# Optimization experiments

Hardware: AMD Instinct MI355X
Metric: run time of the kernel (lower is better)

Reference implementation:

```python
import jax, jax.numpy as jnp
import numpy as np

TAU = 0.07
K = 50
EPS = 1e-8


def _flat_norm(x):
    # [B, C, H, W] -> [B*H*W, C], L2-normalized along C
    B, C = x.shape[0], x.shape[1]
    x = jnp.moveaxis(x, 1, -1).reshape(-1, C)
    n = jnp.linalg.norm(x, axis=-1, keepdims=True)
    return x / jnp.maximum(n, 1e-12)


def setup_inputs() -> dict:
    key = jax.random.key(0)
    ks = jax.random.split(key, 5)
    shp = (2, 128, 64, 64)
    lshp = (2, 4, 64, 64)
    return {
        "input": jax.random.normal(ks[0], shp, dtype=jnp.float32),
        "positive": jax.random.normal(ks[1], shp, dtype=jnp.float32),
        "negative": jax.random.normal(ks[2], shp, dtype=jnp.float32),
        "input_logits": jax.random.normal(ks[3], lshp, dtype=jnp.float32),
        "negative_logits": jax.random.normal(ks[4], lshp, dtype=jnp.float32),
    }


def reference(input, positive, negative, input_logits, negative_logits):
    norm_input = _flat_norm(input)        # [N, C]
    norm_positive = _flat_norm(positive)  # [N, C]
    norm_negative = _flat_norm(negative)  # [N, C]

    # check_input: multi-class logits branch (softmax over class dim, then max)
    in_probs = jax.nn.softmax(input_logits, axis=1)
    neg_probs = jax.nn.softmax(negative_logits, axis=1)
    seg_input = jnp.argmax(in_probs, axis=1).reshape(-1)       # [N] int
    seg_negative = jnp.argmax(neg_probs, axis=1).reshape(-1)   # [N] int
    negative_prob = jnp.max(neg_probs, axis=1).reshape(-1)     # [N] float

    # positive cosine similarity (unit vectors -> dot product)
    pos_sim = jnp.sum(norm_input * norm_positive, axis=-1)     # [N]

    # mask[i, j] = (seg_input[j] != seg_negative[i]) * negative_prob[i]
    diff = (seg_input[None, :] != seg_negative[:, None]).astype(jnp.float16)
    masked = diff.astype(jnp.float32) * negative_prob[:, None]  # [N, N]

    # top-k over dim=0 (negatives) for each input column j -> indices [N, K]
    _, idx = jax.lax.top_k(masked.T, K)                         # [N, K]
    sampled = norm_negative[idx]                                # [N, K, C]

    neg_sim = jnp.einsum('nkc,nc->nk', sampled, norm_input)     # [N, K]
    nominator = jnp.exp(pos_sim / TAU)                          # [N]
    denominator = jnp.sum(jnp.exp(neg_sim / TAU), axis=1) + nominator
    loss = -jnp.mean(jnp.log(nominator / (denominator + EPS)))

    alter_sim = jnp.einsum('nkc,nc->nk', sampled, norm_positive)
    alter_den = jnp.sum(jnp.exp(alter_sim / TAU), axis=1) + nominator
    alter_loss = -jnp.mean(jnp.log(nominator / (alter_den + EPS)))

    return loss + alter_loss
```

## Files before the change

kernel.cpp:

```cpp
#include <hip/hip_runtime.h>
#include <math.h>

#define TAU_INV (1.0f / 0.07f)
#define KSEL 50
#define KPAD 64
#define NPIX 8192
#define CCH 128
#define HWSZ 4096
#define NCLS 4
#define EPSL 1e-8f
#define NBINS 1026
#define PXT 32
#define SROW 132

__global__ void __launch_bounds__(256) prep_kernel(
        const float* __restrict__ input, const float* __restrict__ positive,
        const float* __restrict__ negative,
        const float* __restrict__ ilog, const float* __restrict__ nlog,
        float* __restrict__ ni, float* __restrict__ np_,
        float* __restrict__ nnsel,
        int* __restrict__ perm, int* __restrict__ cnt,
        float* __restrict__ out) {
    __shared__ union {
        struct {
            float tile[CCH][65];
            float partial[4][64];
            float invn[64];
        } a;
        struct {
            unsigned hist[NBINS];
            unsigned coarse[33];
            unsigned long long cand[2048];
            unsigned wsum[4];
            int topk_l[KPAD];
            unsigned above_cnt, cand_cnt;
            int sB, sc0;
        } b;
    } sm;

    int t = threadIdx.x;
    int bid = blockIdx.x;

    if (bid == 0 && t == 0) out[0] = 0.0f;

    if (bid >= NCLS) {
        int blk = bid - NCLS;
        int tensor = blk >> 7, chunk = blk & 127;
        const float* src = (tensor == 0) ? input : positive;
        float*       dst = (tensor == 0) ? ni    : np_;

        int n0 = chunk * 64;
        int b = n0 >> 12, hw0 = n0 & (HWSZ - 1);
        const float* base = src + (size_t)b * CCH * HWSZ + hw0;

        #pragma unroll
        for (int i = 0; i < 8; ++i) {
            int lin = t + i * 256;
            int cc = lin >> 4, hwq = (lin & 15) * 4;
            float4 v = *(const float4*)&base[(size_t)cc * HWSZ + hwq];
            sm.a.tile[cc][hwq + 0] = v.x; sm.a.tile[cc][hwq + 1] = v.y;
            sm.a.tile[cc][hwq + 2] = v.z; sm.a.tile[cc][hwq + 3] = v.w;
        }
        __syncthreads();

        int nof = t & 63, part = t >> 6;
        float s = 0.f;
        #pragma unroll
        for (int j = 0; j < 32; ++j) {
            float v = sm.a.tile[part * 32 + j][nof];
            s += v * v;
        }
        sm.a.partial[part][nof] = s;
        __syncthreads();
        if (t < 64) {
            float tot = sm.a.partial[0][t] + sm.a.partial[1][t] +
                        sm.a.partial[2][t] + sm.a.partial[3][t];
            sm.a.invn[t] = 1.0f / fmaxf(sqrtf(tot), 1e-12f);
        }
        __syncthreads();

        #pragma unroll
        for (int i = 0; i < 8; ++i) {
            int lin = t + i * 256;
            int nf = lin >> 5, cq = (lin & 31) * 4;
            float inv = sm.a.invn[nf];
            float4 o;
            o.x = sm.a.tile[cq + 0][nf] * inv;
            o.y = sm.a.tile[cq + 1][nf] * inv;
            o.z = sm.a.tile[cq + 2][nf] * inv;
            o.w = sm.a.tile[cq + 3][nf] * inv;
            *(float4*)&dst[(size_t)(n0 + nf) * CCH + cq] = o;
        }
        return;
    }

    int c = bid;

    for (int i = t; i < NBINS; i += 256) sm.b.hist[i] = 0;
    if (t < 33) sm.b.coarse[t] = 0;
    if (t == 0) { sm.b.above_cnt = 0; sm.b.cand_cnt = 0; }
    __syncthreads();

    unsigned keys[32];
    unsigned mask = 0u;
    #pragma unroll
    for (int s = 0; s < 8; ++s) {
        int i4 = (t + s * 256) * 4;
        int b = i4 >> 12, hw = i4 & (HWSZ - 1);

        const float* pi = ilog + (size_t)b * NCLS * HWSZ + hw;
        float4 a0 = *(const float4*)&pi[0];
        float4 a1 = *(const float4*)&pi[HWSZ];
        float4 a2 = *(const float4*)&pi[2 * HWSZ];
        float4 a3 = *(const float4*)&pi[3 * HWSZ];
        const float* pn = nlog + (size_t)b * NCLS * HWSZ + hw;
        float4 b0 = *(const float4*)&pn[0];
        float4 b1 = *(const float4*)&pn[HWSZ];
        float4 b2 = *(const float4*)&pn[2 * HWSZ];
        float4 b3 = *(const float4*)&pn[3 * HWSZ];

        const float* A0 = (const float*)&a0; const float* A1 = (const float*)&a1;
        const float* A2 = (const float*)&a2; const float* A3 = (const float*)&a3;
        const float* B0 = (const float*)&b0; const float* B1 = (const float*)&b1;
        const float* B2 = (const float*)&b2; const float* B3 = (const float*)&b3;
        #pragma unroll
        for (int j = 0; j < 4; ++j) {
            float l0 = A0[j], l1 = A1[j], l2 = A2[j], l3 = A3[j];
            int bi = 0; float bv = l0;
            if (l1 > bv) { bv = l1; bi = 1; }
            if (l2 > bv) { bv = l2; bi = 2; }
            if (l3 > bv) { bv = l3; bi = 3; }
            if (bi == c) mask |= (1u << (s * 4 + j));
            float m0 = B0[j], m1 = B1[j], m2 = B2[j], m3 = B3[j];
            int ci = 0; float cv = m0;
            if (m1 > cv) { cv = m1; ci = 1; }
            if (m2 > cv) { cv = m2; ci = 2; }
            if (m3 > cv) { cv = m3; ci = 3; }
            float ssum = expf(m0 - cv) + expf(m1 - cv) + expf(m2 - cv) + expf(m3 - cv);
            float npv = 1.0f / ssum;

            float v = (ci != c) ? npv : 0.0f;
            unsigned key = __float_as_uint(v);
            keys[s * 4 + j] = key;
            int bin = (key < 0x3E800000u) ? 0 : (int)(1u + ((key - 0x3E800000u) >> 14));
            atomicAdd(&sm.b.hist[bin], 1u);
        }
    }

    {
        int cnt_t = __popc(mask);
        int lane = t & 63, wv = t >> 6;
        int x = cnt_t;
        #pragma unroll
        for (int off = 1; off < 64; off <<= 1) {
            int o = __shfl_up(x, off);
            if (lane >= off) x += o;
        }
        if (lane == 63) sm.b.wsum[wv] = (unsigned)x;
        __syncthreads();
        int base = x - cnt_t;
        for (int ww = 0; ww < wv; ++ww) base += (int)sm.b.wsum[ww];
        unsigned mm = mask; int k = 0;
        while (mm) {
            int bit = __ffs(mm) - 1; mm &= (mm - 1);
            int s2 = bit >> 2, j2 = bit & 3;
            perm[c * NPIX + base + k] = (t + s2 * 256) * 4 + j2;
            ++k;
        }
        if (t == 0) cnt[c] = (int)(sm.b.wsum[0] + sm.b.wsum[1] +
                                   sm.b.wsum[2] + sm.b.wsum[3]);
    }
    __syncthreads();

    for (int i = t; i < NBINS; i += 256) atomicAdd(&sm.b.coarse[i >> 5], sm.b.hist[i]);
    __syncthreads();

    if (t == 0) {
        unsigned cum = 0; int j = 32;
        for (; j > 0; --j) {
            unsigned h = sm.b.coarse[j];
            if (cum + h >= KSEL) break;
            cum += h;
        }
        int hi = j * 32 + 31; if (hi > NBINS - 1) hi = NBINS - 1;
        int B = 0;
        for (int b = hi; b >= j * 32; --b) {
            unsigned h = sm.b.hist[b];
            if (cum + h >= KSEL) { B = b; break; }
            cum += h;
        }
        sm.b.sB = B; sm.b.sc0 = (int)cum;
    }
    __syncthreads();
    int B = sm.b.sB, c0 = sm.b.sc0;

    #pragma unroll
    for (int s = 0; s < 8; ++s) {
        #pragma unroll
        for (int j = 0; j < 4; ++j) {
            unsigned key = keys[s * 4 + j];
            int bin = (key < 0x3E800000u) ? 0 : (int)(1u + ((key - 0x3E800000u) >> 14));
            int i = (t + s * 256) * 4 + j;
            if (bin > B) {
                unsigned pos = atomicAdd(&sm.b.above_cnt, 1u);
                sm.b.topk_l[pos] = i;
            } else if (bin == B) {
                unsigned jj = atomicAdd(&sm.b.cand_cnt, 1u);
                if (jj < 2048)
                    sm.b.cand[jj] = ((unsigned long long)key << 32) |
                                    (unsigned long long)(0xFFFFFFFFu - (unsigned)i);
            }
        }
    }
    __syncthreads();

    int m = KSEL - c0;
    int cb = (int)sm.b.cand_cnt; if (cb > 2048) cb = 2048;
    if (t < 64) {
        for (int r = 0; r < m; ++r) {
            unsigned long long best = 0;
            for (int j = t; j < cb; j += 64) {
                unsigned long long v = sm.b.cand[j];
                if (v > best) best = v;
            }
            #pragma unroll
            for (int off = 32; off; off >>= 1) {
                unsigned long long o = __shfl_xor(best, off);
                if (o > best) best = o;
            }
            if (t == 0) sm.b.topk_l[c0 + r] =
                (int)(0xFFFFFFFFu - (unsigned)(best & 0xFFFFFFFFull));
            for (int j = t; j < cb; j += 64)
                if (sm.b.cand[j] == best) sm.b.cand[j] = 0;
        }
    }
    __syncthreads();

    {
        int row = t >> 2;
        int ch0 = (t & 3) * 32;
        if (row < KSEL) {
            int px = sm.b.topk_l[row];
            int b = px >> 12, hw = px & (HWSZ - 1);
            const float* src = negative + (size_t)b * CCH * HWSZ + hw;
            float vals[32]; float ss = 0.f;
            #pragma unroll
            for (int k2 = 0; k2 < 32; ++k2) {
                float v = src[(size_t)(ch0 + k2) * HWSZ];
                vals[k2] = v; ss += v * v;
            }
            ss += __shfl_xor(ss, 1);
            ss += __shfl_xor(ss, 2);
            float inv = 1.0f / fmaxf(sqrtf(ss), 1e-12f);
            float* dst = nnsel + (size_t)(c * KSEL + row) * CCH + ch0;
            #pragma unroll
            for (int k2 = 0; k2 < 32; ++k2) dst[k2] = vals[k2] * inv;
        }
    }
}

__global__ void __launch_bounds__(256) loss_kernel(
        const float* __restrict__ ni, const float* __restrict__ npos,
        const float* __restrict__ nnsel,
        const int* __restrict__ perm, const int* __restrict__ cnt,
        float* __restrict__ out) {
    __shared__ float Sl[KPAD * SROW];
    __shared__ float Xl[PXT * SROW];
    __shared__ float Pl[PXT * SROW];
    __shared__ float bsum[4];

    int c = blockIdx.y;
    int count = cnt[c];
    int start = blockIdx.x * PXT;
    if (start >= count) return;
    int t = threadIdx.x;

    {
        int row = t >> 2;
        int ch0 = (t & 3) * 32;
        float* dst = &Sl[row * SROW + ch0];
        if (row < KSEL) {
            const float* src = nnsel + (size_t)(c * KSEL + row) * CCH + ch0;
            #pragma unroll
            for (int i = 0; i < 8; ++i)
                ((float4*)dst)[i] = ((const float4*)src)[i];
        } else {
            float4 z = make_float4(0.f, 0.f, 0.f, 0.f);
            #pragma unroll
            for (int i = 0; i < 8; ++i)
                ((float4*)dst)[i] = z;
        }
    }
    {
        int row = t >> 3;
        int slot = start + row;
        int px = perm[c * NPIX + ((slot < count) ? slot : start)];
        int ch0 = (t & 7) * 16;
        const float* sx = ni + (size_t)px * CCH + ch0;
        const float* sp = npos + (size_t)px * CCH + ch0;
        float* dx = &Xl[row * SROW + ch0];
        float* dp = &Pl[row * SROW + ch0];
        #pragma unroll
        for (int i = 0; i < 4; ++i) {
            ((float4*)dx)[i] = ((const float4*)sx)[i];
            ((float4*)dp)[i] = ((const float4*)sp)[i];
        }
    }
    __syncthreads();

    int ktid = t & 7, pxid = t >> 3;
    float acc_i[8] = {0.f, 0.f, 0.f, 0.f, 0.f, 0.f, 0.f, 0.f};
    float acc_p[8] = {0.f, 0.f, 0.f, 0.f, 0.f, 0.f, 0.f, 0.f};
    float ps = 0.f;
    const float* Xr = &Xl[pxid * SROW];
    const float* Pr = &Pl[pxid * SROW];

    #pragma unroll 2
    for (int ch = 0; ch < CCH; ch += 4) {
        float4 xv = *(const float4*)&Xr[ch];
        float4 pv = *(const float4*)&Pr[ch];
        ps += xv.x * pv.x + xv.y * pv.y + xv.z * pv.z + xv.w * pv.w;
        #pragma unroll
        for (int r = 0; r < 8; ++r) {
            float4 sv = *(const float4*)&Sl[(ktid + r * 8) * SROW + ch];
            acc_i[r] += sv.x * xv.x + sv.y * xv.y + sv.z * xv.z + sv.w * xv.w;
            acc_p[r] += sv.x * pv.x + sv.y * pv.y + sv.z * pv.z + sv.w * pv.w;
        }
    }

    float si = 0.f, spp = 0.f;
    #pragma unroll
    for (int r = 0; r < 8; ++r) {
        si  += expf(acc_i[r] * TAU_INV);
        spp += expf(acc_p[r] * TAU_INV);
    }
    #pragma unroll
    for (int off = 1; off < 8; off <<= 1) {
        si  += __shfl_xor(si, off);
        spp += __shfl_xor(spp, off);
    }

    float v = 0.f;
    if (ktid == 0 && (start + pxid) < count) {
        si  -= (float)(KPAD - KSEL);
        spp -= (float)(KPAD - KSEL);
        float nom = expf(ps * TAU_INV);
        float li = -logf(nom / (si + nom + EPSL));
        float lp = -logf(nom / (spp + nom + EPSL));
        v = (li + lp) * (1.0f / (float)NPIX);
    }
    v += __shfl_xor(v, 8);
    v += __shfl_xor(v, 16);
    v += __shfl_xor(v, 32);
    int w = t >> 6;
    if ((t & 63) == 0) bsum[w] = v;
    __syncthreads();
    if (t == 0) atomicAdd(out, bsum[0] + bsum[1] + bsum[2] + bsum[3]);
}

extern "C" void kernel_launch(void* const* d_in, const int* in_sizes, int n_in,
                              void* d_out, int out_size, void* d_ws, size_t ws_size,
                              hipStream_t stream) {
    const float* input      = (const float*)d_in[0];
    const float* positive   = (const float*)d_in[1];
    const float* negative   = (const float*)d_in[2];
    const float* in_logits  = (const float*)d_in[3];
    const float* neg_logits = (const float*)d_in[4];
    float* out = (float*)d_out;

    float* ws    = (float*)d_ws;
    float* ni    = ws;
    float* np_   = ws + 1048576;
    float* nnsel = ws + 2097152;
    int*   cnt   = (int*)(ws + 3145728);
    int*   perm  = cnt + 64;

    prep_kernel<<<256 + NCLS, 256, 0, stream>>>(input, positive, negative,
                                                in_logits, neg_logits,
                                                ni, np_, nnsel, perm, cnt, out);
    dim3 lgrid(NPIX / PXT, NCLS);
    loss_kernel<<<lgrid, 256, 0, stream>>>(ni, np_, nnsel, perm, cnt, out);
}
```

Baseline: 109.6 us.

## Fuse input/positive normalization into loss kernel and widen top-k blocks

Removes the separate normalization pass that wrote L2-normalized copies of input and positive to workspace. The loss kernel now gathers raw NCHW values for its selected pixels and normalizes them in registers with a shuffle reduction. This removes a full intermediate write and re-read. The top-k kernel now runs one 1024-thread block per class, with more threads sharing the histogram, scan and negative gather. The trade-off is strided, less coalesced channel reads from NCHW in the loss kernel.

```diff
diff --git a/kernel.cpp b/kernel.cpp
--- a/kernel.cpp
+++ b/kernel.cpp
@@ -13,99 +13,32 @@
 #define PXT 32
 #define SROW 132
 
-__global__ void __launch_bounds__(256) prep_kernel(
-        const float* __restrict__ input, const float* __restrict__ positive,
+__global__ void __launch_bounds__(1024) topk_kernel(
+        const float* __restrict__ ilog, const float* __restrict__ nlog,
         const float* __restrict__ negative,
-        const float* __restrict__ ilog, const float* __restrict__ nlog,
-        float* __restrict__ ni, float* __restrict__ np_,
-        float* __restrict__ nnsel,
-        int* __restrict__ perm, int* __restrict__ cnt,
+        float* __restrict__ nnsel, int* __restrict__ perm, int* __restrict__ cnt,
         float* __restrict__ out) {
-    __shared__ union {
-        struct {
-            float tile[CCH][65];
-            float partial[4][64];
-            float invn[64];
-        } a;
-        struct {
-            unsigned hist[NBINS];
-            unsigned coarse[33];
-            unsigned long long cand[2048];
-            unsigned wsum[4];
-            int topk_l[KPAD];
-            unsigned above_cnt, cand_cnt;
-            int sB, sc0;
-        } b;
-    } sm;
-
-    int t = threadIdx.x;
-    int bid = blockIdx.x;
-
-    if (bid == 0 && t == 0) out[0] = 0.0f;
-
-    if (bid >= NCLS) {
-        int blk = bid - NCLS;
-        int tensor = blk >> 7, chunk = blk & 127;
-        const float* src = (tensor == 0) ? input : positive;
-        float*       dst = (tensor == 0) ? ni    : np_;
-
-        int n0 = chunk * 64;
-        int b = n0 >> 12, hw0 = n0 & (HWSZ - 1);
-        const float* base = src + (size_t)b * CCH * HWSZ + hw0;
-
-        #pragma unroll
-        for (int i = 0; i < 8; ++i) {
-            int lin = t + i * 256;
-            int cc = lin >> 4, hwq = (lin & 15) * 4;
-            float4 v = *(const float4*)&base[(size_t)cc * HWSZ + hwq];
-            sm.a.tile[cc][hwq + 0] = v.x; sm.a.tile[cc][hwq + 1] = v.y;
-            sm.a.tile[cc][hwq + 2] = v.z; sm.a.tile[cc][hwq + 3] = v.w;
-        }
-        __syncthreads();
-
-        int nof = t & 63, part = t >> 6;
-        float s = 0.f;
-        #pragma unroll
-        for (int j = 0; j < 32; ++j) {
-            float v = sm.a.tile[part * 32 + j][nof];
-            s += v * v;
-        }
-        sm.a.partial[part][nof] = s;
-        __syncthreads();
-        if (t < 64) {
-            float tot = sm.a.partial[0][t] + sm.a.partial[1][t] +
-                        sm.a.partial[2][t] + sm.a.partial[3][t];
-            sm.a.invn[t] = 1.0f / fmaxf(sqrtf(tot), 1e-12f);
-        }
-        __syncthreads();
-
-        #pragma unroll
-        for (int i = 0; i < 8; ++i) {
-            int lin = t + i * 256;
-            int nf = lin >> 5, cq = (lin & 31) * 4;
-            float inv = sm.a.invn[nf];
-            float4 o;
-            o.x = sm.a.tile[cq + 0][nf] * inv;
-            o.y = sm.a.tile[cq + 1][nf] * inv;
-            o.z = sm.a.tile[cq + 2][nf] * inv;
-            o.w = sm.a.tile[cq + 3][nf] * inv;
-            *(float4*)&dst[(size_t)(n0 + nf) * CCH + cq] = o;
-        }
-        return;
-    }
-
-    int c = bid;
-
-    for (int i = t; i < NBINS; i += 256) sm.b.hist[i] = 0;
-    if (t < 33) sm.b.coarse[t] = 0;
-    if (t == 0) { sm.b.above_cnt = 0; sm.b.cand_cnt = 0; }
-    __syncthreads();
-
-    unsigned keys[32];
+    __shared__ unsigned hist[NBINS];
+    __shared__ unsigned coarse[33];
+    __shared__ unsigned long long cand[2048];
+    __shared__ unsigned wsum[16];
+    __shared__ int topk_l[KPAD];
+    __shared__ unsigned above_cnt, cand_cnt;
+    __shared__ int sB, sc0;
+
+    int c = blockIdx.x, t = threadIdx.x;
+    if (c == 0 && t == 0) out[0] = 0.0f;
+
+    for (int i = t; i < NBINS; i += 1024) hist[i] = 0;
+    if (t < 33) coarse[t] = 0;
+    if (t == 0) { above_cnt = 0; cand_cnt = 0; }
+    __syncthreads();
+
+    unsigned keys[8];
     unsigned mask = 0u;
     #pragma unroll
-    for (int s = 0; s < 8; ++s) {
-        int i4 = (t + s * 256) * 4;
+    for (int s = 0; s < 2; ++s) {
+        int i4 = (t * 2 + s) * 4;
         int b = i4 >> 12, hw = i4 & (HWSZ - 1);
 
         const float* pi = ilog + (size_t)b * NCLS * HWSZ + hw;
@@ -131,6 +64,7 @@
             if (l2 > bv) { bv = l2; bi = 2; }
             if (l3 > bv) { bv = l3; bi = 3; }
             if (bi == c) mask |= (1u << (s * 4 + j));
+
             float m0 = B0[j], m1 = B1[j], m2 = B2[j], m3 = B3[j];
             int ci = 0; float cv = m0;
             if (m1 > cv) { cv = m1; ci = 1; }
@@ -143,7 +77,7 @@
             unsigned key = __float_as_uint(v);
             keys[s * 4 + j] = key;
             int bin = (key < 0x3E800000u) ? 0 : (int)(1u + ((key - 0x3E800000u) >> 14));
-            atomicAdd(&sm.b.hist[bin], 1u);
+            atomicAdd(&hist[bin], 1u);
         }
     }
 
@@ -156,71 +90,72 @@
             int o = __shfl_up(x, off);
             if (lane >= off) x += o;
         }
-        if (lane == 63) sm.b.wsum[wv] = (unsigned)x;
+        if (lane == 63) wsum[wv] = (unsigned)x;
         __syncthreads();
         int base = x - cnt_t;
-        for (int ww = 0; ww < wv; ++ww) base += (int)sm.b.wsum[ww];
-        unsigned mm = mask; int k = 0;
+        for (int ww = 0; ww < wv; ++ww) base += (int)wsum[ww];
+        unsigned mm = mask;
         while (mm) {
             int bit = __ffs(mm) - 1; mm &= (mm - 1);
-            int s2 = bit >> 2, j2 = bit & 3;
-            perm[c * NPIX + base + k] = (t + s2 * 256) * 4 + j2;
-            ++k;
-        }
-        if (t == 0) cnt[c] = (int)(sm.b.wsum[0] + sm.b.wsum[1] +
-                                   sm.b.wsum[2] + sm.b.wsum[3]);
-    }
-    __syncthreads();
-
-    for (int i = t; i < NBINS; i += 256) atomicAdd(&sm.b.coarse[i >> 5], sm.b.hist[i]);
+            perm[c * NPIX + base] = t * 8 + bit;
+            ++base;
+        }
+        if (t == 0) {
+            int tot = 0;
+            for (int w2 = 0; w2 < 16; ++w2) tot += (int)wsum[w2];
+            cnt[c] = tot;
+        }
+    }
+
+    for (int i = t; i < NBINS; i += 1024) atomicAdd(&coarse[i >> 5], hist[i]);
     __syncthreads();
 
     if (t == 0) {
         unsigned cum = 0; int j = 32;
         for (; j > 0; --j) {
-            unsigned h = sm.b.coarse[j];
+            unsigned h = coarse[j];
             if (cum + h >= KSEL) break;
             cum += h;
         }
         int hi = j * 32 + 31; if (hi > NBINS - 1) hi = NBINS - 1;
         int B = 0;
         for (int b = hi; b >= j * 32; --b) {
-            unsigned h = sm.b.hist[b];
+            unsigned h = hist[b];
             if (cum + h >= KSEL) { B = b; break; }
             cum += h;
         }
-        sm.b.sB = B; sm.b.sc0 = (int)cum;
-    }
-    __syncthreads();
-    int B = sm.b.sB, c0 = sm.b.sc0;
+        sB = B; sc0 = (int)cum;
+    }
+    __syncthreads();
+    int B = sB, c0 = sc0;
 
     #pragma unroll
-    for (int s = 0; s < 8; ++s) {
+    for (int s = 0; s < 2; ++s) {
         #pragma unroll
         for (int j = 0; j < 4; ++j) {
             unsigned key = keys[s * 4 + j];
             int bin = (key < 0x3E800000u) ? 0 : (int)(1u + ((key - 0x3E800000u) >> 14));
-            int i = (t + s * 256) * 4 + j;
+            int i = t * 8 + s * 4 + j;
             if (bin > B) {
-                unsigned pos = atomicAdd(&sm.b.above_cnt, 1u);
-                sm.b.topk_l[pos] = i;
+                unsigned pos = atomicAdd(&above_cnt, 1u);
+                topk_l[pos] = i;
             } else if (bin == B) {
-                unsigned jj = atomicAdd(&sm.b.cand_cnt, 1u);
+                unsigned jj = atomicAdd(&cand_cnt, 1u);
                 if (jj < 2048)
-                    sm.b.cand[jj] = ((unsigned long long)key << 32) |
-                                    (unsigned long long)(0xFFFFFFFFu - (unsigned)i);
+                    cand[jj] = ((unsigned long long)key << 32) |
+                               (unsigned long long)(0xFFFFFFFFu - (unsigned)i);
             }
         }
     }
     __syncthreads();
 
     int m = KSEL - c0;
-    int cb = (int)sm.b.cand_cnt; if (cb > 2048) cb = 2048;
+    int cb = (int)cand_cnt; if (cb > 2048) cb = 2048;
     if (t < 64) {
         for (int r = 0; r < m; ++r) {
             unsigned long long best = 0;
             for (int j = t; j < cb; j += 64) {
-                unsigned long long v = sm.b.cand[j];
+                unsigned long long v = cand[j];
                 if (v > best) best = v;
             }
             #pragma unroll
@@ -228,39 +163,41 @@
                 unsigned long long o = __shfl_xor(best, off);
                 if (o > best) best = o;
             }
-            if (t == 0) sm.b.topk_l[c0 + r] =
+            if (t == 0) topk_l[c0 + r] =
                 (int)(0xFFFFFFFFu - (unsigned)(best & 0xFFFFFFFFull));
             for (int j = t; j < cb; j += 64)
-                if (sm.b.cand[j] == best) sm.b.cand[j] = 0;
+                if (cand[j] == best) cand[j] = 0;
         }
     }
     __syncthreads();
 
     {
-        int row = t >> 2;
-        int ch0 = (t & 3) * 32;
+        int row = t >> 4;
+        int ch0 = (t & 15) * 8;
         if (row < KSEL) {
-            int px = sm.b.topk_l[row];
+            int px = topk_l[row];
             int b = px >> 12, hw = px & (HWSZ - 1);
             const float* src = negative + (size_t)b * CCH * HWSZ + hw;
-            float vals[32]; float ss = 0.f;
-            #pragma unroll
-            for (int k2 = 0; k2 < 32; ++k2) {
-                float v = src[(size_t)(ch0 + k2) * HWSZ];
-                vals[k2] = v; ss += v * v;
+            float vals[8]; float ss = 0.f;
+            #pragma unroll
+            for (int k = 0; k < 8; ++k) {
+                float v = src[(size_t)(ch0 + k) * HWSZ];
+                vals[k] = v; ss += v * v;
             }
             ss += __shfl_xor(ss, 1);
             ss += __shfl_xor(ss, 2);
+            ss += __shfl_xor(ss, 4);
+            ss += __shfl_xor(ss, 8);
             float inv = 1.0f / fmaxf(sqrtf(ss), 1e-12f);
             float* dst = nnsel + (size_t)(c * KSEL + row) * CCH + ch0;
             #pragma unroll
-            for (int k2 = 0; k2 < 32; ++k2) dst[k2] = vals[k2] * inv;
+            for (int k = 0; k < 8; ++k) dst[k] = vals[k] * inv;
         }
     }
 }
 
 __global__ void __launch_bounds__(256) loss_kernel(
-        const float* __restrict__ ni, const float* __restrict__ npos,
+        const float* __restrict__ input, const float* __restrict__ positive,
         const float* __restrict__ nnsel,
         const int* __restrict__ perm, const int* __restrict__ cnt,
         float* __restrict__ out) {
@@ -295,15 +232,34 @@
         int row = t >> 3;
         int slot = start + row;
         int px = perm[c * NPIX + ((slot < count) ? slot : start)];
+        int b = px >> 12, hw = px & (HWSZ - 1);
         int ch0 = (t & 7) * 16;
-        const float* sx = ni + (size_t)px * CCH + ch0;
-        const float* sp = npos + (size_t)px * CCH + ch0;
+        const float* bx = input    + (size_t)b * CCH * HWSZ + hw;
+        const float* bp = positive + (size_t)b * CCH * HWSZ + hw;
+        float xv[16], pv[16];
+        float ssx = 0.f, ssp = 0.f;
+        #pragma unroll
+        for (int k = 0; k < 16; ++k) {
+            float vx = bx[(size_t)(ch0 + k) * HWSZ];
+            float vp = bp[(size_t)(ch0 + k) * HWSZ];
+            xv[k] = vx; ssx += vx * vx;
+            pv[k] = vp; ssp += vp * vp;
+        }
+        ssx += __shfl_xor(ssx, 1); ssp += __shfl_xor(ssp, 1);
+        ssx += __shfl_xor(ssx, 2); ssp += __shfl_xor(ssp, 2);
+        ssx += __shfl_xor(ssx, 4); ssp += __shfl_xor(ssp, 4);
+        float ix = 1.0f / fmaxf(sqrtf(ssx), 1e-12f);
+        float ip = 1.0f / fmaxf(sqrtf(ssp), 1e-12f);
         float* dx = &Xl[row * SROW + ch0];
         float* dp = &Pl[row * SROW + ch0];
         #pragma unroll
         for (int i = 0; i < 4; ++i) {
-            ((float4*)dx)[i] = ((const float4*)sx)[i];
-            ((float4*)dp)[i] = ((const float4*)sp)[i];
+            float4 ox = make_float4(xv[4*i+0]*ix, xv[4*i+1]*ix,
+                                    xv[4*i+2]*ix, xv[4*i+3]*ix);
+            float4 op = make_float4(pv[4*i+0]*ip, pv[4*i+1]*ip,
+                                    pv[4*i+2]*ip, pv[4*i+3]*ip);
+            ((float4*)dx)[i] = ox;
+            ((float4*)dp)[i] = op;
         }
     }
     __syncthreads();
@@ -369,15 +325,13 @@
     float* out = (float*)d_out;
 
     float* ws    = (float*)d_ws;
-    float* ni    = ws;
-    float* np_   = ws + 1048576;
-    float* nnsel = ws + 2097152;
-    int*   cnt   = (int*)(ws + 3145728);
+    float* nnsel = ws;
+    int*   cnt   = (int*)(ws + 32768);
     int*   perm  = cnt + 64;
 
-    prep_kernel<<<256 + NCLS, 256, 0, stream>>>(input, positive, negative,
-                                                in_logits, neg_logits,
-                                                ni, np_, nnsel, perm, cnt, out);
+    topk_kernel<<<NCLS, 1024, 0, stream>>>(in_logits, neg_logits, negative,
+                                           nnsel, perm, cnt, out);
     dim3 lgrid(NPIX / PXT, NCLS);
-    loss_kernel<<<lgrid, 256, 0, stream>>>(ni, np_, nnsel, perm, cnt, out);
+    loss_kernel<<<lgrid, 256, 0, stream>>>(input, positive, nnsel,
+                                           perm, cnt, out);
 }
```

Measured after the change: 104.2 us. 1.05x faster.

## Widen prep blocks to 1024 threads to shorten per-class top-k critical path

Applied to the files above, without the earlier changes.

Launches prep_kernel with 1024 threads per block. The four per-class selection blocks now handle 8 pixels per thread instead of 32, and the negative gather uses 16 threads per row instead of 4. The normalization blocks simply idle 768 of their threads. The workspace offset for cnt/perm moves closer to nnsel. This targets the serial latency of the few class blocks that dominate prep, at the cost of wasted threads in the 256 normalization blocks and lower occupancy per CU.

```diff
diff --git a/kernel.cpp b/kernel.cpp
--- a/kernel.cpp
+++ b/kernel.cpp
@@ -13,7 +13,7 @@
 #define PXT 32
 #define SROW 132
 
-__global__ void __launch_bounds__(256) prep_kernel(
+__global__ void __launch_bounds__(1024) prep_kernel(
         const float* __restrict__ input, const float* __restrict__ positive,
         const float* __restrict__ negative,
         const float* __restrict__ ilog, const float* __restrict__ nlog,
@@ -31,7 +31,7 @@
             unsigned hist[NBINS];
             unsigned coarse[33];
             unsigned long long cand[2048];
-            unsigned wsum[4];
+            unsigned wsum[16];
             int topk_l[KPAD];
             unsigned above_cnt, cand_cnt;
             int sB, sc0;
@@ -41,8 +41,6 @@
     int t = threadIdx.x;
     int bid = blockIdx.x;
 
-    if (bid == 0 && t == 0) out[0] = 0.0f;
-
     if (bid >= NCLS) {
         int blk = bid - NCLS;
         int tensor = blk >> 7, chunk = blk & 127;
@@ -53,24 +51,28 @@
         int b = n0 >> 12, hw0 = n0 & (HWSZ - 1);
         const float* base = src + (size_t)b * CCH * HWSZ + hw0;
 
-        #pragma unroll
-        for (int i = 0; i < 8; ++i) {
-            int lin = t + i * 256;
-            int cc = lin >> 4, hwq = (lin & 15) * 4;
-            float4 v = *(const float4*)&base[(size_t)cc * HWSZ + hwq];
-            sm.a.tile[cc][hwq + 0] = v.x; sm.a.tile[cc][hwq + 1] = v.y;
-            sm.a.tile[cc][hwq + 2] = v.z; sm.a.tile[cc][hwq + 3] = v.w;
+        if (t < 256) {
+            #pragma unroll
+            for (int i = 0; i < 8; ++i) {
+                int lin = t + i * 256;
+                int cc = lin >> 4, hwq = (lin & 15) * 4;
+                float4 v = *(const float4*)&base[(size_t)cc * HWSZ + hwq];
+                sm.a.tile[cc][hwq + 0] = v.x; sm.a.tile[cc][hwq + 1] = v.y;
+                sm.a.tile[cc][hwq + 2] = v.z; sm.a.tile[cc][hwq + 3] = v.w;
+            }
         }
         __syncthreads();
 
-        int nof = t & 63, part = t >> 6;
-        float s = 0.f;
-        #pragma unroll
-        for (int j = 0; j < 32; ++j) {
-            float v = sm.a.tile[part * 32 + j][nof];
-            s += v * v;
-        }
-        sm.a.partial[part][nof] = s;
+        if (t < 256) {
+            int nof = t & 63, part = t >> 6;
+            float s = 0.f;
+            #pragma unroll
+            for (int j = 0; j < 32; ++j) {
+                float v = sm.a.tile[part * 32 + j][nof];
+                s += v * v;
+            }
+            sm.a.partial[part][nof] = s;
+        }
         __syncthreads();
         if (t < 64) {
             float tot = sm.a.partial[0][t] + sm.a.partial[1][t] +
@@ -79,33 +81,36 @@
         }
         __syncthreads();
 
-        #pragma unroll
-        for (int i = 0; i < 8; ++i) {
-            int lin = t + i * 256;
-            int nf = lin >> 5, cq = (lin & 31) * 4;
-            float inv = sm.a.invn[nf];
-            float4 o;
-            o.x = sm.a.tile[cq + 0][nf] * inv;
-            o.y = sm.a.tile[cq + 1][nf] * inv;
-            o.z = sm.a.tile[cq + 2][nf] * inv;
-            o.w = sm.a.tile[cq + 3][nf] * inv;
-            *(float4*)&dst[(size_t)(n0 + nf) * CCH + cq] = o;
+        if (t < 256) {
+            #pragma unroll
+            for (int i = 0; i < 8; ++i) {
+                int lin = t + i * 256;
+                int nf = lin >> 5, cq = (lin & 31) * 4;
+                float inv = sm.a.invn[nf];
+                float4 o;
+                o.x = sm.a.tile[cq + 0][nf] * inv;
+                o.y = sm.a.tile[cq + 1][nf] * inv;
+                o.z = sm.a.tile[cq + 2][nf] * inv;
+                o.w = sm.a.tile[cq + 3][nf] * inv;
+                *(float4*)&dst[(size_t)(n0 + nf) * CCH + cq] = o;
+            }
         }
         return;
     }
 
     int c = bid;
-
-    for (int i = t; i < NBINS; i += 256) sm.b.hist[i] = 0;
+    if (c == 0 && t == 0) out[0] = 0.0f;
+
+    for (int i = t; i < NBINS; i += 1024) sm.b.hist[i] = 0;
     if (t < 33) sm.b.coarse[t] = 0;
     if (t == 0) { sm.b.above_cnt = 0; sm.b.cand_cnt = 0; }
     __syncthreads();
 
-    unsigned keys[32];
+    unsigned keys[8];
     unsigned mask = 0u;
     #pragma unroll
-    for (int s = 0; s < 8; ++s) {
-        int i4 = (t + s * 256) * 4;
+    for (int s = 0; s < 2; ++s) {
+        int i4 = (t * 2 + s) * 4;
         int b = i4 >> 12, hw = i4 & (HWSZ - 1);
 
         const float* pi = ilog + (size_t)b * NCLS * HWSZ + hw;
@@ -131,6 +136,7 @@
             if (l2 > bv) { bv = l2; bi = 2; }
             if (l3 > bv) { bv = l3; bi = 3; }
             if (bi == c) mask |= (1u << (s * 4 + j));
+
             float m0 = B0[j], m1 = B1[j], m2 = B2[j], m3 = B3[j];
             int ci = 0; float cv = m0;
             if (m1 > cv) { cv = m1; ci = 1; }
@@ -160,19 +166,20 @@
         __syncthreads();
         int base = x - cnt_t;
         for (int ww = 0; ww < wv; ++ww) base += (int)sm.b.wsum[ww];
-        unsigned mm = mask; int k = 0;
+        unsigned mm = mask;
         while (mm) {
             int bit = __ffs(mm) - 1; mm &= (mm - 1);
-            int s2 = bit >> 2, j2 = bit & 3;
-            perm[c * NPIX + base + k] = (t + s2 * 256) * 4 + j2;
-            ++k;
-        }
-        if (t == 0) cnt[c] = (int)(sm.b.wsum[0] + sm.b.wsum[1] +
-                                   sm.b.wsum[2] + sm.b.wsum[3]);
-    }
-    __syncthreads();
-
-    for (int i = t; i < NBINS; i += 256) atomicAdd(&sm.b.coarse[i >> 5], sm.b.hist[i]);
+            perm[c * NPIX + base] = t * 8 + bit;
+            ++base;
+        }
+        if (t == 0) {
+            int tot = 0;
+            for (int w2 = 0; w2 < 16; ++w2) tot += (int)sm.b.wsum[w2];
+            cnt[c] = tot;
+        }
+    }
+
+    for (int i = t; i < NBINS; i += 1024) atomicAdd(&sm.b.coarse[i >> 5], sm.b.hist[i]);
     __syncthreads();
 
     if (t == 0) {
@@ -195,12 +202,12 @@
     int B = sm.b.sB, c0 = sm.b.sc0;
 
     #pragma unroll
-    for (int s = 0; s < 8; ++s) {
+    for (int s = 0; s < 2; ++s) {
         #pragma unroll
         for (int j = 0; j < 4; ++j) {
             unsigned key = keys[s * 4 + j];
             int bin = (key < 0x3E800000u) ? 0 : (int)(1u + ((key - 0x3E800000u) >> 14));
-            int i = (t + s * 256) * 4 + j;
+            int i = t * 8 + s * 4 + j;
             if (bin > B) {
                 unsigned pos = atomicAdd(&sm.b.above_cnt, 1u);
                 sm.b.topk_l[pos] = i;
@@ -237,24 +244,26 @@
     __syncthreads();
 
     {
-        int row = t >> 2;
-        int ch0 = (t & 3) * 32;
+        int row = t >> 4;
+        int ch0 = (t & 15) * 8;
         if (row < KSEL) {
             int px = sm.b.topk_l[row];
             int b = px >> 12, hw = px & (HWSZ - 1);
             const float* src = negative + (size_t)b * CCH * HWSZ + hw;
-            float vals[32]; float ss = 0.f;
-            #pragma unroll
-            for (int k2 = 0; k2 < 32; ++k2) {
-                float v = src[(size_t)(ch0 + k2) * HWSZ];
-                vals[k2] = v; ss += v * v;
+            float vals[8]; float ss = 0.f;
+            #pragma unroll
+            for (int k = 0; k < 8; ++k) {
+                float v = src[(size_t)(ch0 + k) * HWSZ];
+                vals[k] = v; ss += v * v;
             }
             ss += __shfl_xor(ss, 1);
             ss += __shfl_xor(ss, 2);
+            ss += __shfl_xor(ss, 4);
+            ss += __shfl_xor(ss, 8);
             float inv = 1.0f / fmaxf(sqrtf(ss), 1e-12f);
             float* dst = nnsel + (size_t)(c * KSEL + row) * CCH + ch0;
             #pragma unroll
-            for (int k2 = 0; k2 < 32; ++k2) dst[k2] = vals[k2] * inv;
+            for (int k = 0; k < 8; ++k) dst[k] = vals[k] * inv;
         }
     }
 }
@@ -372,12 +381,12 @@
     float* ni    = ws;
     float* np_   = ws + 1048576;
     float* nnsel = ws + 2097152;
-    int*   cnt   = (int*)(ws + 3145728);
+    int*   cnt   = (int*)(ws + 2097152 + 32768);
     int*   perm  = cnt + 64;
 
-    prep_kernel<<<256 + NCLS, 256, 0, stream>>>(input, positive, negative,
-                                                in_logits, neg_logits,
-                                                ni, np_, nnsel, perm, cnt, out);
+    prep_kernel<<<256 + NCLS, 1024, 0, stream>>>(input, positive, negative,
+                                                 in_logits, neg_logits,
+                                                 ni, np_, nnsel, perm, cnt, out);
     dim3 lgrid(NPIX / PXT, NCLS);
     loss_kernel<<<lgrid, 256, 0, stream>>>(ni, np_, nnsel, perm, cnt, out);
 }
```

New measurement: 105.6 us. 3.6% less time.
